# Kernel optimization log

Hardware: AMD Instinct MI355X
Metric: run time of the kernel (lower is better)

Reference implementation:

```python
import jax, jax.numpy as jnp
import numpy as np

NUM_PLANES = 65
EMBED_DIM = 64   # must equal NUM_PLANES - 1: Linear is applied over the 'e' axis
ANT_DIM = 128
B = 4


def conv2d(x, w, b):
    # NCHW conv, 3x3, stride 1, padding 1 (== SAME)
    y = jax.lax.conv_general_dilated(x, w, window_strides=(1, 1), padding='SAME',
                                     dimension_numbers=('NCHW', 'OIHW', 'NCHW'))
    return y + b[None, :, None, None]


def setup_inputs() -> dict:
    key = jax.random.key(0)
    ks = jax.random.split(key, 8)
    D = EMBED_DIM
    return {
        'x': jax.random.normal(ks[0], (B, NUM_PLANES, 8, 8), jnp.float32),
        'piece_emb': jax.random.normal(ks[1], (NUM_PLANES - 1, D), jnp.float32),
        'pos_emb': jax.random.normal(ks[2], (64, D), jnp.float32),
        'w1': jax.random.normal(ks[3], (D // 2, D), jnp.float32) / np.sqrt(D).astype(np.float32),
        'b1': jnp.zeros((D // 2,), jnp.float32),
        'w2': jax.random.normal(ks[4], (1, D // 2), jnp.float32) / np.sqrt(D // 2).astype(np.float32),
        'b2': jnp.zeros((1,), jnp.float32),
        'conv1_w': jax.random.normal(ks[5], (ANT_DIM, NUM_PLANES, 3, 3), jnp.float32) * 0.05,
        'conv1_b': jnp.zeros((ANT_DIM,), jnp.float32),
        'conv2_w': jax.random.normal(ks[6], (ANT_DIM, ANT_DIM, 3, 3), jnp.float32) * 0.05,
        'conv2_b': jnp.zeros((ANT_DIM,), jnp.float32),
    }


def reference(x, piece_emb, pos_emb, w1, b1, w2, b2, conv1_w, conv1_b, conv2_w, conv2_b):
    # --- SpatialEmbeddingLayer ---
    # se[b,c,h,w,d,e] = x[b,c,h,w] * piece_emb[e,d] + pos_emb[h*8+w, d]
    se = jnp.einsum('bchw,ed->bchwde', x[:, :-1], piece_emb)
    se = se + pos_emb.reshape(1, 1, 8, 8, EMBED_DIM)[..., None]  # broadcast over e
    # --- PieceRelationshipModule ---
    rel = jnp.einsum('bchwde,bshwde->bcshwe', se, se)            # [B,C,C,8,8,E]
    h = jax.nn.relu(jnp.einsum('...e,fe->...f', rel, w1) + b1)   # [B,C,C,8,8,E//2]
    enc = jnp.einsum('...f,of->...o', h, w2) + b2                # [B,C,C,8,8,1]
    rel_out = enc.sum(axis=(2, 3, 5))                            # [B,C,8]
    # --- AnticipationMechanism ---
    ant = conv2d(jax.nn.relu(conv2d(x, conv1_w, conv1_b)), conv2_w, conv2_b)  # [B,ANT_DIM,8,8]
    return (se, rel_out, ant)
```

## Files before the change

kernel.cpp:

```cpp
#include <hip/hip_runtime.h>

using f4 = __attribute__((ext_vector_type(4))) float;

#define REL_OFF 67108864ull
#define ANT_OFF 67110912ull

#define WS_PT 0
#define WS_A1 4096
#define WS_BT 4128
#define WS_CT 6176
#define WS_Y1 8224

__global__ __launch_bounds__(1024) void precompute_kernel(
    const float* __restrict__ P,
    const float* __restrict__ Q,
    const float* __restrict__ w1,
    const float* __restrict__ b1,
    float* __restrict__ ws) {
  __shared__ float Plds[4096];
  __shared__ float Ptl[4096];
  __shared__ float Qlds[4096];
  __shared__ float W1P[2048];
  __shared__ float A[64], Cc[64], s1[32];
  int t = threadIdx.x;
  for (int i = t; i < 4096; i += 1024) { Plds[i] = P[i]; Qlds[i] = Q[i]; }
  __syncthreads();
  for (int i = t; i < 4096; i += 1024) {
    int d = i >> 6, e = i & 63;
    Ptl[i] = Plds[(e << 6) + d];
  }
  if (t < 64) {
    float s = 0.f;
    for (int d = 0; d < 64; ++d) { float p = Plds[(t << 6) + d]; s = fmaf(p, p, s); }
    A[t] = s;
  } else if (t < 128) {
    int hw = t - 64; float s = 0.f;
    for (int d = 0; d < 64; ++d) { float q = Qlds[(hw << 6) + d]; s = fmaf(q, q, s); }
    Cc[hw] = s;
  } else if (t < 160) {
    int f = t - 128; float s = 0.f;
    for (int e = 0; e < 64; ++e) s += w1[(f << 6) + e];
    s1[f] = s;
  }
  __syncthreads();
  for (int i = t; i < 4096; i += 1024) ws[WS_PT + i] = Ptl[i];
  if (t < 32) {
    float s = 0.f;
    for (int e = 0; e < 64; ++e) s = fmaf(A[e], w1[(t << 6) + e], s);
    ws[WS_A1 + t] = s;
  }
  for (int i = t; i < 2048; i += 1024) {
    int f = i >> 6, d = i & 63;
    float s = 0.f;
    for (int e = 0; e < 64; ++e) s = fmaf(w1[(f << 6) + e], Ptl[(d << 6) + e], s);
    W1P[i] = s;
  }
  __syncthreads();
  for (int i = t; i < 2048; i += 1024) {
    int f = i >> 6, hw = i & 63;
    float s = 0.f;
    for (int d = 0; d < 64; ++d) s = fmaf(W1P[(f << 6) + d], Qlds[(hw << 6) + d], s);
    ws[WS_BT + i] = s;
    ws[WS_CT + i] = fmaf(Cc[hw], s1[f], b1[f]);
  }
}

__global__ __launch_bounds__(256) void se_kernel(
    const float* __restrict__ x,
    const float* __restrict__ pt,
    const float* __restrict__ q,
    float* __restrict__ out) {
  int blk = blockIdx.x;
  int hw = blk & 63, bc = blk >> 6;
  int b = bc >> 6, c = bc & 63;
  float xv = x[((b * 65 + c) << 6) + hw];
  int t = threadIdx.x;
  const f4* pt4 = (const f4*)pt;
  f4* out4 = (f4*)(out + ((size_t)blk << 12));
#pragma unroll
  for (int k = 0; k < 4; ++k) {
    int i4 = t + (k << 8);
    int d = i4 >> 4;
    float qd = q[(hw << 6) + d];
    f4 p = pt4[i4];
    f4 r;
    r[0] = fmaf(xv, p[0], qd);
    r[1] = fmaf(xv, p[1], qd);
    r[2] = fmaf(xv, p[2], qd);
    r[3] = fmaf(xv, p[3], qd);
    __builtin_nontemporal_store(r, out4 + i4);
  }
}

__global__ __launch_bounds__(256) void rel_kernel(
    const float* __restrict__ x,
    const float* __restrict__ bt,
    const float* __restrict__ ct,
    const float* __restrict__ a1,
    const float* __restrict__ w2,
    const float* __restrict__ b2,
    float* __restrict__ out) {
  __shared__ float xl[4096];
  __shared__ float a1l[32], w2l[32];
  __shared__ float red[8];
  int t = threadIdx.x;
  int bc = blockIdx.x; int b = bc >> 6, c = bc & 63;
  for (int i = t; i < 4096; i += 256) {
    int s = i >> 6, hw = i & 63;
    xl[i] = x[((b * 65 + s) << 6) + hw];
  }
  if (t < 32) { a1l[t] = a1[t]; w2l[t] = w2[t]; }
  if (t < 8) red[t] = 0.f;
  int hw = t & 63, sg = t >> 6;
  float btr[32], ctr[32];
#pragma unroll
  for (int f = 0; f < 32; ++f) { btr[f] = bt[(f << 6) + hw]; ctr[f] = ct[(f << 6) + hw]; }
  __syncthreads();
  float b2v = b2[0];
  float xc = xl[(c << 6) + hw];
  float partial = 0.f;
  for (int s = sg; s < 64; s += 4) {
    float xs = xl[(s << 6) + hw];
    float u = xc * xs, v = xc + xs;
    float acc = b2v;
#pragma unroll
    for (int f = 0; f < 32; ++f) {
      float tt = fmaf(u, a1l[f], fmaf(v, btr[f], ctr[f]));
      acc = fmaf(fmaxf(tt, 0.f), w2l[f], acc);
    }
    partial += acc;
  }
  atomicAdd(&red[hw & 7], partial);
  __syncthreads();
  if (t < 8) out[bc * 8 + t] = red[t];
}

__global__ __launch_bounds__(256) void conv1_kernel(
    const float* __restrict__ x, const float* __restrict__ w,
    const float* __restrict__ bias, float* __restrict__ y1) {
  __shared__ float xp[6500];
  int blk = blockIdx.x;
  int b = blk >> 5, chunk = blk & 31;
  int t = threadIdx.x;
  for (int i = t; i < 6500; i += 256) xp[i] = 0.f;
  __syncthreads();
  for (int i = t; i < 4160; i += 256) {
    int ci = i >> 6, hw = i & 63;
    xp[ci * 100 + ((hw >> 3) + 1) * 10 + (hw & 7) + 1] = x[((b * 65 + ci) << 6) + hw];
  }
  __syncthreads();
  int hw = t & 63, wv = t >> 6;
  int h = hw >> 3, ww = hw & 7;
  int co = (chunk << 2) + wv;
  float acc = bias[co];
  const float* wc = w + co * 585;
  for (int ci = 0; ci < 65; ++ci) {
    const float* xr = xp + ci * 100 + h * 10 + ww;
    const float* wr = wc + ci * 9;
#pragma unroll
    for (int dy = 0; dy < 3; ++dy)
#pragma unroll
      for (int dx = 0; dx < 3; ++dx)
        acc = fmaf(xr[dy * 10 + dx], wr[dy * 3 + dx], acc);
  }
  y1[(((b << 7) + co) << 6) + hw] = fmaxf(acc, 0.f);
}

__global__ __launch_bounds__(256) void conv2_kernel(
    const float* __restrict__ y1, const float* __restrict__ w,
    const float* __restrict__ bias, float* __restrict__ out) {
  __shared__ float yp[12800];
  int blk = blockIdx.x;
  int b = blk >> 5, chunk = blk & 31;
  int t = threadIdx.x;
  for (int i = t; i < 12800; i += 256) yp[i] = 0.f;
  __syncthreads();
  for (int i = t; i < 8192; i += 256) {
    int ci = i >> 6, hw = i & 63;
    yp[ci * 100 + ((hw >> 3) + 1) * 10 + (hw & 7) + 1] = y1[(((b << 7) + ci) << 6) + hw];
  }
  __syncthreads();
  int hw = t & 63, wv = t >> 6;
  int h = hw >> 3, ww = hw & 7;
  int co = (chunk << 2) + wv;
  float acc = bias[co];
  const float* wc = w + co * 1152;
  for (int ci = 0; ci < 128; ++ci) {
    const float* xr = yp + ci * 100 + h * 10 + ww;
    const float* wr = wc + ci * 9;
#pragma unroll
    for (int dy = 0; dy < 3; ++dy)
#pragma unroll
      for (int dx = 0; dx < 3; ++dx)
        acc = fmaf(xr[dy * 10 + dx], wr[dy * 3 + dx], acc);
  }
  out[(((b << 7) + co) << 6) + hw] = acc;
}

extern "C" void kernel_launch(void* const* d_in, const int* in_sizes, int n_in,
                              void* d_out, int out_size, void* d_ws, size_t ws_size,
                              hipStream_t stream) {
  const float* x     = (const float*)d_in[0];
  const float* piece = (const float*)d_in[1];
  const float* pos   = (const float*)d_in[2];
  const float* w1    = (const float*)d_in[3];
  const float* b1    = (const float*)d_in[4];
  const float* w2    = (const float*)d_in[5];
  const float* b2    = (const float*)d_in[6];
  const float* c1w   = (const float*)d_in[7];
  const float* c1b   = (const float*)d_in[8];
  const float* c2w   = (const float*)d_in[9];
  const float* c2b   = (const float*)d_in[10];
  float* out = (float*)d_out;
  float* ws  = (float*)d_ws;

  precompute_kernel<<<1, 1024, 0, stream>>>(piece, pos, w1, b1, ws);
  se_kernel<<<16384, 256, 0, stream>>>(x, ws + WS_PT, pos, out);
  conv1_kernel<<<128, 256, 0, stream>>>(x, c1w, c1b, ws + WS_Y1);
  conv2_kernel<<<128, 256, 0, stream>>>(ws + WS_Y1, c2w, c2b, out + ANT_OFF);
  rel_kernel<<<256, 256, 0, stream>>>(x, ws + WS_BT, ws + WS_CT, ws + WS_A1, w2, b2, out + REL_OFF);
}
```

Measured before the change: 356.2 us.

## Merge five launches into two heterogeneous kernels and drop precompute serialization

Folds the precompute, se and conv1 work into one launch, with block ranges assigned to each role, and folds conv2 and the relationship reduction into a second launch. The se blocks now transpose piece_emb into LDS themselves, padded to avoid bank conflicts, and each writes four hw positions, which cuts the grid from 16384 blocks to 4096. The single-block precompute runs alongside the other work instead of serializing ahead of everything. The cost is that every se block reloads P into LDS, and the heterogeneous blocks share one LDS allocation sized for the largest role, which can lower occupancy for the smaller roles.

```diff
diff --git a/kernel.cpp b/kernel.cpp
--- a/kernel.cpp
+++ b/kernel.cpp
@@ -5,196 +5,191 @@
 #define REL_OFF 67108864ull
 #define ANT_OFF 67110912ull
 
-#define WS_PT 0
-#define WS_A1 4096
-#define WS_BT 4128
-#define WS_CT 6176
-#define WS_Y1 8224
-
-__global__ __launch_bounds__(1024) void precompute_kernel(
+#define WS_A1 0
+#define WS_BT 32
+#define WS_CT 2080
+#define WS_Y1 4128
+
+#define C1_BLOCKS 128
+#define PRE_BLOCK 128
+#define SE_BASE   129
+#define SE_BLOCKS 4096
+
+__global__ __launch_bounds__(256) void k2_se_conv1_pre(
+    const float* __restrict__ x,
     const float* __restrict__ P,
     const float* __restrict__ Q,
     const float* __restrict__ w1,
     const float* __restrict__ b1,
-    float* __restrict__ ws) {
-  __shared__ float Plds[4096];
-  __shared__ float Ptl[4096];
-  __shared__ float Qlds[4096];
-  __shared__ float W1P[2048];
-  __shared__ float A[64], Cc[64], s1[32];
-  int t = threadIdx.x;
-  for (int i = t; i < 4096; i += 1024) { Plds[i] = P[i]; Qlds[i] = Q[i]; }
-  __syncthreads();
-  for (int i = t; i < 4096; i += 1024) {
-    int d = i >> 6, e = i & 63;
-    Ptl[i] = Plds[(e << 6) + d];
-  }
-  if (t < 64) {
-    float s = 0.f;
-    for (int d = 0; d < 64; ++d) { float p = Plds[(t << 6) + d]; s = fmaf(p, p, s); }
-    A[t] = s;
-  } else if (t < 128) {
-    int hw = t - 64; float s = 0.f;
-    for (int d = 0; d < 64; ++d) { float q = Qlds[(hw << 6) + d]; s = fmaf(q, q, s); }
-    Cc[hw] = s;
-  } else if (t < 160) {
-    int f = t - 128; float s = 0.f;
-    for (int e = 0; e < 64; ++e) s += w1[(f << 6) + e];
-    s1[f] = s;
-  }
-  __syncthreads();
-  for (int i = t; i < 4096; i += 1024) ws[WS_PT + i] = Ptl[i];
-  if (t < 32) {
-    float s = 0.f;
-    for (int e = 0; e < 64; ++e) s = fmaf(A[e], w1[(t << 6) + e], s);
-    ws[WS_A1 + t] = s;
-  }
-  for (int i = t; i < 2048; i += 1024) {
-    int f = i >> 6, d = i & 63;
-    float s = 0.f;
-    for (int e = 0; e < 64; ++e) s = fmaf(w1[(f << 6) + e], Ptl[(d << 6) + e], s);
-    W1P[i] = s;
-  }
-  __syncthreads();
-  for (int i = t; i < 2048; i += 1024) {
-    int f = i >> 6, hw = i & 63;
-    float s = 0.f;
-    for (int d = 0; d < 64; ++d) s = fmaf(W1P[(f << 6) + d], Qlds[(hw << 6) + d], s);
-    ws[WS_BT + i] = s;
-    ws[WS_CT + i] = fmaf(Cc[hw], s1[f], b1[f]);
+    const float* __restrict__ c1w, const float* __restrict__ c1b,
+    float* __restrict__ out, float* __restrict__ ws) {
+  __shared__ float lds[6528];
+  int bid = blockIdx.x, t = threadIdx.x;
+
+  if (bid >= SE_BASE) {
+    int blk = bid - SE_BASE;
+    int hwq = blk & 15, bc = blk >> 4;
+    int b = bc >> 6, c = bc & 63;
+    for (int i = t; i < 4096; i += 256) lds[(i >> 6) * 65 + (i & 63)] = P[i];
+    float xv[4];
+    const float* xr = x + ((b * 65 + c) << 6) + (hwq << 2);
+#pragma unroll
+    for (int m = 0; m < 4; ++m) xv[m] = xr[m];
+    __syncthreads();
+    f4* outb = (f4*)out + ((size_t)bc << 16) + ((size_t)hwq << 12);
+#pragma unroll
+    for (int m = 0; m < 4; ++m) {
+      int hw = (hwq << 2) + m;
+#pragma unroll
+      for (int k = 0; k < 4; ++k) {
+        int i4 = t + (k << 8);
+        int d = i4 >> 4, j = i4 & 15;
+        float qd = Q[(hw << 6) + d];
+        f4 r;
+#pragma unroll
+        for (int kk = 0; kk < 4; ++kk)
+          r[kk] = fmaf(xv[m], lds[(((j << 2) + kk) * 65) + d], qd);
+        __builtin_nontemporal_store(r, outb + (m << 10) + i4);
+      }
+    }
+  } else if (bid < C1_BLOCKS) {
+    float* xp = lds;
+    int b = bid >> 5, chunk = bid & 31;
+    for (int i = t; i < 6500; i += 256) xp[i] = 0.f;
+    __syncthreads();
+    for (int i = t; i < 4160; i += 256) {
+      int ci = i >> 6, hw = i & 63;
+      xp[ci * 100 + ((hw >> 3) + 1) * 10 + (hw & 7) + 1] = x[((b * 65 + ci) << 6) + hw];
+    }
+    __syncthreads();
+    int hw = t & 63, wv = t >> 6;
+    int h = hw >> 3, ww = hw & 7;
+    int co = (chunk << 2) + wv;
+    float acc = c1b[co];
+    const float* wc = c1w + co * 585;
+    for (int ci = 0; ci < 65; ++ci) {
+      const float* xr2 = xp + ci * 100 + h * 10 + ww;
+      const float* wr = wc + ci * 9;
+#pragma unroll
+      for (int dy = 0; dy < 3; ++dy)
+#pragma unroll
+        for (int dx = 0; dx < 3; ++dx)
+          acc = fmaf(xr2[dy * 10 + dx], wr[dy * 3 + dx], acc);
+    }
+    ws[WS_Y1 + (((b << 7) + co) << 6) + hw] = fmaxf(acc, 0.f);
+  } else {
+    float* W1P = lds;
+    float* A   = lds + 2048;
+    float* Cc  = lds + 2112;
+    float* s1  = lds + 2176;
+    if (t < 64) {
+      float s = 0.f;
+      for (int d = 0; d < 64; ++d) { float p = P[(t << 6) + d]; s = fmaf(p, p, s); }
+      A[t] = s;
+    } else if (t < 128) {
+      int hw = t - 64; float s = 0.f;
+      for (int d = 0; d < 64; ++d) { float q = Q[(hw << 6) + d]; s = fmaf(q, q, s); }
+      Cc[hw] = s;
+    } else if (t < 160) {
+      int f = t - 128; float s = 0.f;
+      for (int e = 0; e < 64; ++e) s += w1[(f << 6) + e];
+      s1[f] = s;
+    }
+    for (int i = t; i < 2048; i += 256) {
+      int f = i >> 6, d = i & 63;
+      float s = 0.f;
+      for (int e = 0; e < 64; ++e) s = fmaf(w1[(f << 6) + e], P[(e << 6) + d], s);
+      W1P[i] = s;
+    }
+    __syncthreads();
+    if (t < 32) {
+      float s = 0.f;
+      for (int e = 0; e < 64; ++e) s = fmaf(A[e], w1[(t << 6) + e], s);
+      ws[WS_A1 + t] = s;
+    }
+    for (int i = t; i < 2048; i += 256) {
+      int f = i >> 6, hw = i & 63;
+      float s = 0.f;
+      for (int d = 0; d < 64; ++d) s = fmaf(W1P[(f << 6) + d], Q[(hw << 6) + d], s);
+      ws[WS_BT + i] = s;
+      ws[WS_CT + i] = fmaf(Cc[hw], s1[f], b1[f]);
+    }
   }
 }
 
-__global__ __launch_bounds__(256) void se_kernel(
+__global__ __launch_bounds__(256) void k3_conv2_rel(
     const float* __restrict__ x,
-    const float* __restrict__ pt,
-    const float* __restrict__ q,
+    const float* __restrict__ ws,
+    const float* __restrict__ w2, const float* __restrict__ b2,
+    const float* __restrict__ c2w, const float* __restrict__ c2b,
     float* __restrict__ out) {
-  int blk = blockIdx.x;
-  int hw = blk & 63, bc = blk >> 6;
-  int b = bc >> 6, c = bc & 63;
-  float xv = x[((b * 65 + c) << 6) + hw];
-  int t = threadIdx.x;
-  const f4* pt4 = (const f4*)pt;
-  f4* out4 = (f4*)(out + ((size_t)blk << 12));
-#pragma unroll
-  for (int k = 0; k < 4; ++k) {
-    int i4 = t + (k << 8);
-    int d = i4 >> 4;
-    float qd = q[(hw << 6) + d];
-    f4 p = pt4[i4];
-    f4 r;
-    r[0] = fmaf(xv, p[0], qd);
-    r[1] = fmaf(xv, p[1], qd);
-    r[2] = fmaf(xv, p[2], qd);
-    r[3] = fmaf(xv, p[3], qd);
-    __builtin_nontemporal_store(r, out4 + i4);
+  __shared__ float lds[12800];
+  int bid = blockIdx.x, t = threadIdx.x;
+
+  if (bid < 128) {
+    float* yp = lds;
+    int b = bid >> 5, chunk = bid & 31;
+    const float* y1 = ws + WS_Y1;
+    for (int i = t; i < 12800; i += 256) yp[i] = 0.f;
+    __syncthreads();
+    for (int i = t; i < 8192; i += 256) {
+      int ci = i >> 6, hw = i & 63;
+      yp[ci * 100 + ((hw >> 3) + 1) * 10 + (hw & 7) + 1] = y1[(((b << 7) + ci) << 6) + hw];
+    }
+    __syncthreads();
+    int hw = t & 63, wv = t >> 6;
+    int h = hw >> 3, ww = hw & 7;
+    int co = (chunk << 2) + wv;
+    float acc = c2b[co];
+    const float* wc = c2w + co * 1152;
+    for (int ci = 0; ci < 128; ++ci) {
+      const float* xr = yp + ci * 100 + h * 10 + ww;
+      const float* wr = wc + ci * 9;
+#pragma unroll
+      for (int dy = 0; dy < 3; ++dy)
+#pragma unroll
+        for (int dx = 0; dx < 3; ++dx)
+          acc = fmaf(xr[dy * 10 + dx], wr[dy * 3 + dx], acc);
+    }
+    out[ANT_OFF + (((b << 7) + co) << 6) + hw] = acc;
+  } else {
+    float* xl  = lds;
+    float* a1l = lds + 4096;
+    float* w2l = lds + 4128;
+    float* red = lds + 4160;
+    int bc = bid - 128; int b = bc >> 6, c = bc & 63;
+    for (int i = t; i < 4096; i += 256) {
+      int s = i >> 6, hw = i & 63;
+      xl[i] = x[((b * 65 + s) << 6) + hw];
+    }
+    if (t < 32) { a1l[t] = ws[WS_A1 + t]; w2l[t] = w2[t]; }
+    if (t < 8) red[t] = 0.f;
+    int hw = t & 63, sg = t >> 6;
+    float btr[32], ctr[32];
+#pragma unroll
+    for (int f = 0; f < 32; ++f) {
+      btr[f] = ws[WS_BT + (f << 6) + hw];
+      ctr[f] = ws[WS_CT + (f << 6) + hw];
+    }
+    __syncthreads();
+    float b2v = b2[0];
+    float xc = xl[(c << 6) + hw];
+    float partial = 0.f;
+    for (int s = sg; s < 64; s += 4) {
+      float xs = xl[(s << 6) + hw];
+      float u = xc * xs, v = xc + xs;
+      float acc = b2v;
+#pragma unroll
+      for (int f = 0; f < 32; ++f) {
+        float tt = fmaf(u, a1l[f], fmaf(v, btr[f], ctr[f]));
+        acc = fmaf(fmaxf(tt, 0.f), w2l[f], acc);
+      }
+      partial += acc;
+    }
+    atomicAdd(&red[hw & 7], partial);
+    __syncthreads();
+    if (t < 8) out[REL_OFF + bc * 8 + t] = red[t];
   }
-}
-
-__global__ __launch_bounds__(256) void rel_kernel(
-    const float* __restrict__ x,
-    const float* __restrict__ bt,
-    const float* __restrict__ ct,
-    const float* __restrict__ a1,
-    const float* __restrict__ w2,
-    const float* __restrict__ b2,
-    float* __restrict__ out) {
-  __shared__ float xl[4096];
-  __shared__ float a1l[32], w2l[32];
-  __shared__ float red[8];
-  int t = threadIdx.x;
-  int bc = blockIdx.x; int b = bc >> 6, c = bc & 63;
-  for (int i = t; i < 4096; i += 256) {
-    int s = i >> 6, hw = i & 63;
-    xl[i] = x[((b * 65 + s) << 6) + hw];
-  }
-  if (t < 32) { a1l[t] = a1[t]; w2l[t] = w2[t]; }
-  if (t < 8) red[t] = 0.f;
-  int hw = t & 63, sg = t >> 6;
-  float btr[32], ctr[32];
-#pragma unroll
-  for (int f = 0; f < 32; ++f) { btr[f] = bt[(f << 6) + hw]; ctr[f] = ct[(f << 6) + hw]; }
-  __syncthreads();
-  float b2v = b2[0];
-  float xc = xl[(c << 6) + hw];
-  float partial = 0.f;
-  for (int s = sg; s < 64; s += 4) {
-    float xs = xl[(s << 6) + hw];
-    float u = xc * xs, v = xc + xs;
-    float acc = b2v;
-#pragma unroll
-    for (int f = 0; f < 32; ++f) {
-      float tt = fmaf(u, a1l[f], fmaf(v, btr[f], ctr[f]));
-      acc = fmaf(fmaxf(tt, 0.f), w2l[f], acc);
-    }
-    partial += acc;
-  }
-  atomicAdd(&red[hw & 7], partial);
-  __syncthreads();
-  if (t < 8) out[bc * 8 + t] = red[t];
-}
-
-__global__ __launch_bounds__(256) void conv1_kernel(
-    const float* __restrict__ x, const float* __restrict__ w,
-    const float* __restrict__ bias, float* __restrict__ y1) {
-  __shared__ float xp[6500];
-  int blk = blockIdx.x;
-  int b = blk >> 5, chunk = blk & 31;
-  int t = threadIdx.x;
-  for (int i = t; i < 6500; i += 256) xp[i] = 0.f;
-  __syncthreads();
-  for (int i = t; i < 4160; i += 256) {
-    int ci = i >> 6, hw = i & 63;
-    xp[ci * 100 + ((hw >> 3) + 1) * 10 + (hw & 7) + 1] = x[((b * 65 + ci) << 6) + hw];
-  }
-  __syncthreads();
-  int hw = t & 63, wv = t >> 6;
-  int h = hw >> 3, ww = hw & 7;
-  int co = (chunk << 2) + wv;
-  float acc = bias[co];
-  const float* wc = w + co * 585;
-  for (int ci = 0; ci < 65; ++ci) {
-    const float* xr = xp + ci * 100 + h * 10 + ww;
-    const float* wr = wc + ci * 9;
-#pragma unroll
-    for (int dy = 0; dy < 3; ++dy)
-#pragma unroll
-      for (int dx = 0; dx < 3; ++dx)
-        acc = fmaf(xr[dy * 10 + dx], wr[dy * 3 + dx], acc);
-  }
-  y1[(((b << 7) + co) << 6) + hw] = fmaxf(acc, 0.f);
-}
-
-__global__ __launch_bounds__(256) void conv2_kernel(
-    const float* __restrict__ y1, const float* __restrict__ w,
-    const float* __restrict__ bias, float* __restrict__ out) {
-  __shared__ float yp[12800];
-  int blk = blockIdx.x;
-  int b = blk >> 5, chunk = blk & 31;
-  int t = threadIdx.x;
-  for (int i = t; i < 12800; i += 256) yp[i] = 0.f;
-  __syncthreads();
-  for (int i = t; i < 8192; i += 256) {
-    int ci = i >> 6, hw = i & 63;
-    yp[ci * 100 + ((hw >> 3) + 1) * 10 + (hw & 7) + 1] = y1[(((b << 7) + ci) << 6) + hw];
-  }
-  __syncthreads();
-  int hw = t & 63, wv = t >> 6;
-  int h = hw >> 3, ww = hw & 7;
-  int co = (chunk << 2) + wv;
-  float acc = bias[co];
-  const float* wc = w + co * 1152;
-  for (int ci = 0; ci < 128; ++ci) {
-    const float* xr = yp + ci * 100 + h * 10 + ww;
-    const float* wr = wc + ci * 9;
-#pragma unroll
-    for (int dy = 0; dy < 3; ++dy)
-#pragma unroll
-      for (int dx = 0; dx < 3; ++dx)
-        acc = fmaf(xr[dy * 10 + dx], wr[dy * 3 + dx], acc);
-  }
-  out[(((b << 7) + co) << 6) + hw] = acc;
 }
 
 extern "C" void kernel_launch(void* const* d_in, const int* in_sizes, int n_in,
@@ -214,9 +209,7 @@
   float* out = (float*)d_out;
   float* ws  = (float*)d_ws;
 
-  precompute_kernel<<<1, 1024, 0, stream>>>(piece, pos, w1, b1, ws);
-  se_kernel<<<16384, 256, 0, stream>>>(x, ws + WS_PT, pos, out);
-  conv1_kernel<<<128, 256, 0, stream>>>(x, c1w, c1b, ws + WS_Y1);
-  conv2_kernel<<<128, 256, 0, stream>>>(ws + WS_Y1, c2w, c2b, out + ANT_OFF);
-  rel_kernel<<<256, 256, 0, stream>>>(x, ws + WS_BT, ws + WS_CT, ws + WS_A1, w2, b2, out + REL_OFF);
+  k2_se_conv1_pre<<<SE_BASE + SE_BLOCKS, 256, 0, stream>>>(
+      x, piece, pos, w1, b1, c1w, c1b, out, ws);
+  k3_conv2_rel<<<384, 256, 0, stream>>>(x, ws, w2, b2, c2w, c2b, out);
 }
```

After: 311.9 us. 12.4% less time.
